# Kernel tuning notes

Hardware: AMD Instinct MI355X
Metric: run time of the kernel (lower is better)

The kernel has to match this reference:

```python
import jax, jax.numpy as jnp
import numpy as np

B = 524288        # batch
W = 64            # window_size


def setup_inputs() -> dict:
    key = jax.random.key(0)
    k1, k2, k3 = jax.random.split(key, 3)
    x = jax.random.normal(k1, (B, W), dtype=jnp.float32)
    theta = 0.01 * jax.random.normal(k2, (W, 2), dtype=jnp.float32)
    w = jax.random.normal(k3, (1, 1), dtype=jnp.float32)
    b = jnp.zeros((1,), dtype=jnp.float32)
    return {"x": x, "theta": theta, "w": w, "b": b}


def _expval_z(x, theta):
    """Single-qubit re-uploading circuit: for each t, RX(x_t) RY(th_t0) RZ(th_t1)
    applied to |0>, then <Z>. State carried as two complex amplitudes [B]."""
    bsz = x.shape[0]
    s0 = jnp.ones((bsz,), dtype=jnp.complex64)
    s1 = jnp.zeros((bsz,), dtype=jnp.complex64)

    def step(state, inp):
        s0, s1 = state
        xt, th = inp                      # xt: [B], th: [2]
        # RX(xt): [[c, -i s], [-i s, c]], half-angle
        c = jnp.cos(0.5 * xt).astype(jnp.complex64)
        s = jnp.sin(0.5 * xt).astype(jnp.complex64)
        n0 = c * s0 - 1j * s * s1
        n1 = -1j * s * s0 + c * s1
        # RY(th[0]): [[cy, -sy], [sy, cy]]
        cy = jnp.cos(0.5 * th[0]).astype(jnp.complex64)
        sy = jnp.sin(0.5 * th[0]).astype(jnp.complex64)
        m0 = cy * n0 - sy * n1
        m1 = sy * n0 + cy * n1
        # RZ(th[1]): diag(e^{-i th/2}, e^{+i th/2})
        p = jnp.exp(-0.5j * th[1].astype(jnp.complex64))
        return (p * m0, jnp.conj(p) * m1), None

    (s0, s1), _ = jax.lax.scan(step, (s0, s1), (x.T, theta))  # xs leading dim W
    # <Z> = |s0|^2 - |s1|^2 (real)
    return ((s0 * jnp.conj(s0) - s1 * jnp.conj(s1)).real).astype(jnp.float32)


def reference(x, theta, w, b):
    z = _expval_z(x, theta)               # [B]
    return z * w[0, 0] + b[0]             # Linear(1,1) readout, squeezed -> [B]
```

## Files before the change

### kernel.cpp

```cpp
#include <hip/hip_runtime.h>

#define WSZ   64
#define CHUNK 32
#define BLOCK 256
#define PAD   (CHUNK + 1)

__device__ __forceinline__ void hw_sincos(float ang, float& s, float& c) {
    const float INV2PI = 0.15915494309189535f;
    float r = ang * INV2PI;
    s = __builtin_amdgcn_sinf(r);
    c = __builtin_amdgcn_cosf(r);
}

__global__ __launch_bounds__(BLOCK) void sq_reupload_kernel(
    const float* __restrict__ x,
    const float* __restrict__ theta,
    const float* __restrict__ w,
    const float* __restrict__ bias,
    float* __restrict__ out)
{
    __shared__ float4 tA[WSZ];
    __shared__ float4 tB[WSZ];
    __shared__ float  xs[BLOCK * PAD];

    const int tid = threadIdx.x;
    const int tlo = tid & 7;
    const int thi = tid >> 3;

    const size_t row0 = (size_t)blockIdx.x * BLOCK;
    const float* xblk = x + row0 * WSZ;

    float4 r0[8], r1[8];
    #pragma unroll
    for (int j = 0; j < 8; ++j) {
        int rr = thi + j * 32;
        r0[j] = *reinterpret_cast<const float4*>(xblk + (size_t)rr * WSZ + tlo * 4);
    }

    if (tid < WSZ) {
        float a = theta[2 * tid + 0];
        float b = theta[2 * tid + 1];
        float sa = sinf(a), ca = cosf(a);
        float sb = sinf(b), cb = cosf(b);
        tA[tid] = make_float4(cb * ca, -sb, cb * sa, sb * ca);
        tB[tid] = make_float4(cb, sb * sa, -sa, ca);
    }

    #pragma unroll
    for (int j = 0; j < 8; ++j) {
        int rr = thi + j * 32;
        float* p = &xs[rr * PAD + tlo * 4];
        p[0] = r0[j].x; p[1] = r0[j].y; p[2] = r0[j].z; p[3] = r0[j].w;
    }

    #pragma unroll
    for (int j = 0; j < 8; ++j) {
        int rr = thi + j * 32;
        r1[j] = *reinterpret_cast<const float4*>(xblk + (size_t)rr * WSZ + CHUNK + tlo * 4);
    }

    __syncthreads();

    float vx = 0.0f, vy = 0.0f, vz = 1.0f;
    const int rbase = tid * PAD;

    #pragma unroll
    for (int t = 0; t < CHUNK; ++t) {
        float xt = xs[rbase + t];
        float s, c;
        hw_sincos(xt, s, c);
        float y1 = c * vy - s * vz;
        float z1 = s * vy + c * vz;
        float4 A = tA[t];
        float4 Bv = tB[t];
        float nx = A.x * vx + A.y * y1 + A.z * z1;
        float ny = A.w * vx + Bv.x * y1 + Bv.y * z1;
        float nz = Bv.z * vx + Bv.w * z1;
        vx = nx; vy = ny; vz = nz;
    }

    __syncthreads();

    #pragma unroll
    for (int j = 0; j < 8; ++j) {
        int rr = thi + j * 32;
        float* p = &xs[rr * PAD + tlo * 4];
        p[0] = r1[j].x; p[1] = r1[j].y; p[2] = r1[j].z; p[3] = r1[j].w;
    }

    __syncthreads();

    #pragma unroll
    for (int t = 0; t < CHUNK; ++t) {
        float xt = xs[rbase + t];
        float s, c;
        hw_sincos(xt, s, c);
        float y1 = c * vy - s * vz;
        float z1 = s * vy + c * vz;
        float4 A = tA[CHUNK + t];
        float4 Bv = tB[CHUNK + t];
        float nx = A.x * vx + A.y * y1 + A.z * z1;
        float ny = A.w * vx + Bv.x * y1 + Bv.y * z1;
        float nz = Bv.z * vx + Bv.w * z1;
        vx = nx; vy = ny; vz = nz;
    }

    out[row0 + tid] = vz * w[0] + bias[0];
}

extern "C" void kernel_launch(void* const* d_in, const int* in_sizes, int n_in,
                              void* d_out, int out_size, void* d_ws, size_t ws_size,
                              hipStream_t stream) {
    const float* x     = (const float*)d_in[0];
    const float* theta = (const float*)d_in[1];
    const float* w     = (const float*)d_in[2];
    const float* b     = (const float*)d_in[3];
    float* out = (float*)d_out;

    int nrows = out_size;
    int grid  = (nrows + BLOCK - 1) / BLOCK;
    sq_reupload_kernel<<<grid, BLOCK, 0, stream>>>(x, theta, w, b, out);
}
```

Baseline: 35.09 us.

## Precompute theta coefficients in a separate kernel and pipeline x in smaller chunks

```diff
diff --git a/kernel.cpp b/kernel.cpp
--- a/kernel.cpp
+++ b/kernel.cpp
@@ -1,108 +1,90 @@
 #include <hip/hip_runtime.h>
 
-#define WSZ   64
-#define CHUNK 32
-#define BLOCK 256
-#define PAD   (CHUNK + 1)
+#define WSZ    64
+#define BLOCK  256
+#define CHUNK  16
+#define PAD    (CHUNK + 1)
+#define NCHUNK (WSZ / CHUNK)
 
-__device__ __forceinline__ void hw_sincos(float ang, float& s, float& c) {
-    const float INV2PI = 0.15915494309189535f;
-    float r = ang * INV2PI;
-    s = __builtin_amdgcn_sinf(r);
-    c = __builtin_amdgcn_cosf(r);
+__global__ void coef_kernel(const float* __restrict__ theta, float* __restrict__ coef) {
+    int t = threadIdx.x;
+    if (t < WSZ) {
+        float a = theta[2 * t + 0];
+        float b = theta[2 * t + 1];
+        float sa = sinf(a), ca = cosf(a);
+        float sb = sinf(b), cb = cosf(b);
+        float4* c4 = reinterpret_cast<float4*>(coef);
+        c4[2 * t + 0] = make_float4(cb * ca, -sb, cb * sa, sb * ca);
+        c4[2 * t + 1] = make_float4(cb, sb * sa, -sa, ca);
+    }
 }
 
-__global__ __launch_bounds__(BLOCK) void sq_reupload_kernel(
+__global__ __launch_bounds__(BLOCK) void sq_main(
     const float* __restrict__ x,
-    const float* __restrict__ theta,
+    const float* __restrict__ coef,
     const float* __restrict__ w,
     const float* __restrict__ bias,
     float* __restrict__ out)
 {
-    __shared__ float4 tA[WSZ];
-    __shared__ float4 tB[WSZ];
-    __shared__ float  xs[BLOCK * PAD];
+    __shared__ float xs[BLOCK * PAD];
 
     const int tid = threadIdx.x;
-    const int tlo = tid & 7;
-    const int thi = tid >> 3;
-
+    const int tlo = tid & 3;
+    const int thi = tid >> 2;
     const size_t row0 = (size_t)blockIdx.x * BLOCK;
     const float* xblk = x + row0 * WSZ;
+    const float INV2PI = 0.15915494309189535f;
 
-    float4 r0[8], r1[8];
+    float4 rcur[4], rnxt[4];
     #pragma unroll
-    for (int j = 0; j < 8; ++j) {
-        int rr = thi + j * 32;
-        r0[j] = *reinterpret_cast<const float4*>(xblk + (size_t)rr * WSZ + tlo * 4);
+    for (int j = 0; j < 4; ++j) {
+        int rr = thi + j * 64;
+        rcur[j] = *reinterpret_cast<const float4*>(xblk + (size_t)rr * WSZ + tlo * 4);
     }
-
-    if (tid < WSZ) {
-        float a = theta[2 * tid + 0];
-        float b = theta[2 * tid + 1];
-        float sa = sinf(a), ca = cosf(a);
-        float sb = sinf(b), cb = cosf(b);
-        tA[tid] = make_float4(cb * ca, -sb, cb * sa, sb * ca);
-        tB[tid] = make_float4(cb, sb * sa, -sa, ca);
-    }
-
-    #pragma unroll
-    for (int j = 0; j < 8; ++j) {
-        int rr = thi + j * 32;
-        float* p = &xs[rr * PAD + tlo * 4];
-        p[0] = r0[j].x; p[1] = r0[j].y; p[2] = r0[j].z; p[3] = r0[j].w;
-    }
-
-    #pragma unroll
-    for (int j = 0; j < 8; ++j) {
-        int rr = thi + j * 32;
-        r1[j] = *reinterpret_cast<const float4*>(xblk + (size_t)rr * WSZ + CHUNK + tlo * 4);
-    }
-
-    __syncthreads();
 
     float vx = 0.0f, vy = 0.0f, vz = 1.0f;
     const int rbase = tid * PAD;
 
     #pragma unroll
-    for (int t = 0; t < CHUNK; ++t) {
-        float xt = xs[rbase + t];
-        float s, c;
-        hw_sincos(xt, s, c);
-        float y1 = c * vy - s * vz;
-        float z1 = s * vy + c * vz;
-        float4 A = tA[t];
-        float4 Bv = tB[t];
-        float nx = A.x * vx + A.y * y1 + A.z * z1;
-        float ny = A.w * vx + Bv.x * y1 + Bv.y * z1;
-        float nz = Bv.z * vx + Bv.w * z1;
-        vx = nx; vy = ny; vz = nz;
-    }
+    for (int c = 0; c < NCHUNK; ++c) {
+        if (c < NCHUNK - 1) {
+            #pragma unroll
+            for (int j = 0; j < 4; ++j) {
+                int rr = thi + j * 64;
+                rnxt[j] = *reinterpret_cast<const float4*>(
+                    xblk + (size_t)rr * WSZ + (c + 1) * CHUNK + tlo * 4);
+            }
+        }
+        #pragma unroll
+        for (int j = 0; j < 4; ++j) {
+            int rr = thi + j * 64;
+            float* p = &xs[rr * PAD + tlo * 4];
+            p[0] = rcur[j].x * INV2PI;
+            p[1] = rcur[j].y * INV2PI;
+            p[2] = rcur[j].z * INV2PI;
+            p[3] = rcur[j].w * INV2PI;
+        }
+        __syncthreads();
 
-    __syncthreads();
+        #pragma unroll
+        for (int t = 0; t < CHUNK; ++t) {
+            float r = xs[rbase + t];
+            float s  = __builtin_amdgcn_sinf(r);
+            float co = __builtin_amdgcn_cosf(r);
+            const float* cf = coef + c * (CHUNK * 8) + t * 8;
+            float y1 = co * vy - s * vz;
+            float z1 = s * vy + co * vz;
+            float nx = cf[0] * vx + cf[1] * y1 + cf[2] * z1;
+            float ny = cf[3] * vx + cf[4] * y1 + cf[5] * z1;
+            float nz = cf[6] * vx + cf[7] * z1;
+            vx = nx; vy = ny; vz = nz;
+        }
+        __syncthreads();
 
-    #pragma unroll
-    for (int j = 0; j < 8; ++j) {
-        int rr = thi + j * 32;
-        float* p = &xs[rr * PAD + tlo * 4];
-        p[0] = r1[j].x; p[1] = r1[j].y; p[2] = r1[j].z; p[3] = r1[j].w;
-    }
-
-    __syncthreads();
-
-    #pragma unroll
-    for (int t = 0; t < CHUNK; ++t) {
-        float xt = xs[rbase + t];
-        float s, c;
-        hw_sincos(xt, s, c);
-        float y1 = c * vy - s * vz;
-        float z1 = s * vy + c * vz;
-        float4 A = tA[CHUNK + t];
-        float4 Bv = tB[CHUNK + t];
-        float nx = A.x * vx + A.y * y1 + A.z * z1;
-        float ny = A.w * vx + Bv.x * y1 + Bv.y * z1;
-        float nz = Bv.z * vx + Bv.w * z1;
-        vx = nx; vy = ny; vz = nz;
+        if (c < NCHUNK - 1) {
+            #pragma unroll
+            for (int j = 0; j < 4; ++j) rcur[j] = rnxt[j];
+        }
     }
 
     out[row0 + tid] = vz * w[0] + bias[0];
@@ -115,9 +97,12 @@
     const float* theta = (const float*)d_in[1];
     const float* w     = (const float*)d_in[2];
     const float* b     = (const float*)d_in[3];
-    float* out = (float*)d_out;
+    float* out  = (float*)d_out;
+    float* coef = (float*)d_ws;
+
+    coef_kernel<<<1, 64, 0, stream>>>(theta, coef);
 
     int nrows = out_size;
     int grid  = (nrows + BLOCK - 1) / BLOCK;
-    sq_reupload_kernel<<<grid, BLOCK, 0, stream>>>(x, theta, w, b, out);
+    sq_main<<<grid, BLOCK, 0, stream>>>(x, coef, w, b, out);
 }
```

Result: slower. 42.86 us (+22.1%).
